# Performance work log

Measured on AMD Instinct MI355X. Metric: run time of the kernel, lower is better.

The kernel has to match this reference:

```python
import jax, jax.numpy as jnp
import numpy as np

B, U, L, H = 2048, 512, 32, 64  # batch, num_units, latent_dim, hidden


def setup_inputs() -> dict:
    key = jax.random.key(0)
    ks = jax.random.split(key, 17)
    s = 0.05  # weight scale
    inp = {
        "x": jax.random.normal(ks[0], (B, U), dtype=jnp.float32),
        # encoder: U -> 64 -> 64 -> 64 -> L
        "We1": jax.random.normal(ks[1], (U, H), jnp.float32) * s,
        "be1": jnp.zeros((H,), jnp.float32),
        "We2": jax.random.normal(ks[2], (H, H), jnp.float32) * s,
        "be2": jnp.zeros((H,), jnp.float32),
        "We3": jax.random.normal(ks[3], (H, H), jnp.float32) * s,
        "be3": jnp.zeros((H,), jnp.float32),
        "We4": jax.random.normal(ks[4], (H, L), jnp.float32) * s,
        "be4": jnp.zeros((L,), jnp.float32),
        # U disjoint decoders, weights stacked along unit axis: L -> 64 -> 64 -> 64 -> 1
        "Wd1": jax.random.normal(ks[5], (U, L, H), jnp.float32) * s,
        "bd1": jnp.zeros((U, H), jnp.float32),
        "Wd2": jax.random.normal(ks[6], (U, H, H), jnp.float32) * s,
        "bd2": jnp.zeros((U, H), jnp.float32),
        "Wd3": jax.random.normal(ks[7], (U, H, H), jnp.float32) * s,
        "bd3": jnp.zeros((U, H), jnp.float32),
        "Wd4": jax.random.normal(ks[8], (U, H), jnp.float32) * s,  # last layer out_dim=1, squeezed
        "bd4": jnp.zeros((U,), jnp.float32),
    }
    return inp


def reference(x, We1, be1, We2, be2, We3, be3, We4, be4,
              Wd1, bd1, Wd2, bd2, Wd3, bd3, Wd4, bd4):
    # shared encoder MLP: [B, U] -> [B, L]
    z = jax.nn.relu(x @ We1 + be1)
    z = jax.nn.relu(z @ We2 + be2)
    z = jax.nn.relu(z @ We3 + be3)
    z = z @ We4 + be4  # [B, L]
    # all U decoders batched as grouped GEMMs: [B, L] -> [B, U]
    h = jax.nn.relu(jnp.einsum('bl,ulh->buh', z, Wd1) + bd1)   # [B, U, H]
    h = jax.nn.relu(jnp.einsum('buh,uhk->buk', h, Wd2) + bd2)  # [B, U, H]
    h = jax.nn.relu(jnp.einsum('buh,uhk->buk', h, Wd3) + bd3)  # [B, U, H]
    out = jnp.einsum('buh,uh->bu', h, Wd4) + bd4               # [B, U]
    return out
```

## Files before the change

kernel.cpp:

```cpp
#include <hip/hip_runtime.h>
#include <hip/hip_bf16.h>
#include <hip/hip_fp16.h>
#include <stdint.h>

#define NB 2048
#define NU 512
#define NL 32
#define NH 64

typedef float    f4    __attribute__((ext_vector_type(4)));
typedef uint32_t u32x4 __attribute__((ext_vector_type(4)));
typedef _Float16 h8    __attribute__((ext_vector_type(8)));
typedef _Float16 h2    __attribute__((ext_vector_type(2)));

__device__ __forceinline__ f4 mfma16h(u32x4 a, u32x4 b, f4 c) {
    return __builtin_amdgcn_mfma_f32_16x16x32_f16(
        __builtin_bit_cast(h8, a), __builtin_bit_cast(h8, b), c, 0, 0, 0);
}

__device__ __forceinline__ uint32_t pk2h(float a, float b) {
    uint32_t la = (uint32_t)__half_as_ushort(__float2half_rn(a));
    uint32_t hb = (uint32_t)__half_as_ushort(__float2half_rn(b));
    return la | (hb << 16);
}

__device__ __forceinline__ uint32_t pk_rtz(float e, float o) {
    return __builtin_bit_cast(uint32_t, __builtin_amdgcn_cvt_pkrtz(e, o));
}

__device__ __forceinline__ uint32_t pk_relu(float e, float o) {
    uint32_t r = pk_rtz(e, o);
    asm("v_pk_max_f16 %0, %1, 0" : "=v"(r) : "v"(r));
    return r;
}

__device__ __forceinline__ float dot2(uint32_t a, uint32_t b, float c) {
    return __builtin_amdgcn_fdot2(__builtin_bit_cast(h2, a),
                                  __builtin_bit_cast(h2, b), c, false);
}

__global__ __launch_bounds__(512)
void enc_kernel(const float* __restrict__ x,
                const float* __restrict__ We1, const float* __restrict__ be1,
                const float* __restrict__ We2, const float* __restrict__ be2,
                const float* __restrict__ We3, const float* __restrict__ be3,
                const float* __restrict__ We4, const float* __restrict__ be4,
                uint32_t* __restrict__ zpk)
{
    const int RE = 8;
    __shared__ float xs[RE][512];
    __shared__ float ws[128 * 64];
    __shared__ float h[RE][NH];
    __shared__ float h2s[RE][NH];

    const int t  = threadIdx.x;
    const int r0 = blockIdx.x * RE;

    {
        const f4* xv  = (const f4*)(x + (size_t)r0 * 512);
        f4*       xsv = (f4*)&xs[0][0];
        for (int i = t; i < RE * 512 / 4; i += 512) xsv[i] = xv[i];
    }

    const int j = t & 63;
    const int w = t >> 6;

    float acc0 = be1[j];
    for (int kc = 0; kc < 512; kc += 128) {
        __syncthreads();
        const f4* wv  = (const f4*)(We1 + (size_t)kc * 64);
        f4*       wsv = (f4*)ws;
        for (int i = t; i < 128 * 64 / 4; i += 512) wsv[i] = wv[i];
        __syncthreads();
        #pragma unroll 8
        for (int k = 0; k < 128; ++k)
            acc0 = fmaf(xs[w][kc + k], ws[k * 64 + j], acc0);
    }
    acc0 = fmaxf(acc0, 0.f);
    __syncthreads();
    h[w][j] = acc0;
    __syncthreads();

    acc0 = be2[j];
    #pragma unroll
    for (int k = 0; k < 64; ++k)
        acc0 = fmaf(h[w][k], We2[k * 64 + j], acc0);
    acc0 = fmaxf(acc0, 0.f);
    h2s[w][j] = acc0;
    __syncthreads();

    acc0 = be3[j];
    #pragma unroll
    for (int k = 0; k < 64; ++k)
        acc0 = fmaf(h2s[w][k], We3[k * 64 + j], acc0);
    acc0 = fmaxf(acc0, 0.f);
    h[w][j] = acc0;
    __syncthreads();

    if (t < 256) {
        const int j4  = t & 31;
        const int row = t >> 5;
        float acc = be4[j4];
        #pragma unroll
        for (int k = 0; k < 64; ++k)
            acc = fmaf(h[row][k], We4[k * 32 + j4], acc);
        float nb = __shfl_xor(acc, 1);
        if ((j4 & 1) == 0)
            zpk[(size_t)(r0 + row) * 16 + (j4 >> 1)] = pk2h(acc, nb);
    }
}

template <int K2>
__device__ __forceinline__ void stageW(const float* __restrict__ g,
                                       uint32_t (*dst)[68], int t)
{
    for (int g4 = t; g4 < K2 * 16; g4 += 256) {
        const int k2 = g4 >> 4, c4 = (g4 & 15) << 2;
        f4 a = *(const f4*)(g + (size_t)(2 * k2) * NH + c4);
        f4 b = *(const f4*)(g + (size_t)(2 * k2 + 1) * NH + c4);
        u32x4 p;
        p[0] = pk2h(a[0], b[0]);
        p[1] = pk2h(a[1], b[1]);
        p[2] = pk2h(a[2], b[2]);
        p[3] = pk2h(a[3], b[3]);
        *(u32x4*)&dst[k2][c4] = p;
    }
}

__global__ __launch_bounds__(256)
void dec_kernel(const uint32_t* __restrict__ zpk,
                const float* __restrict__ Wd1, const float* __restrict__ bd1,
                const float* __restrict__ Wd2, const float* __restrict__ bd2,
                const float* __restrict__ Wd3, const float* __restrict__ bd3,
                const float* __restrict__ Wd4, const float* __restrict__ bd4,
                float* __restrict__ out)
{
    __shared__ uint32_t wpk1[16][68];
    __shared__ uint32_t wpk2[32][68];
    __shared__ uint32_t wpk3[72][68];
    __shared__ float bsh[3][NH];
    __shared__ float w4s[NH];

    const int bid  = blockIdx.x;
    const int half = bid >> 9;
    const int ub   = bid & 511;
    const int u = ((ub & 7) << 4) | (((ub >> 3) & 3) << 7) | (ub >> 5);
    const int t = threadIdx.x;

    stageW<16>(Wd1 + (size_t)u * NL * NH, wpk1, t);
    stageW<32>(Wd2 + (size_t)u * NH * NH, wpk2, t);
    stageW<32>(Wd3 + (size_t)u * NH * NH, wpk3, t);
    if (t < NH) {
        bsh[0][t] = bd1[(size_t)u * NH + t];
        bsh[1][t] = bd2[(size_t)u * NH + t];
        bsh[2][t] = bd3[(size_t)u * NH + t];
        w4s[t]    = Wd4[(size_t)u * NH + t];
    }
    __syncthreads();

    const int w  = t >> 6;
    const int lr = t & 15;
    const int lg = (t & 63) >> 4;
    const float b4 = bd4[u];

    int cperm[4];
    #pragma unroll
    for (int mt = 0; mt < 4; ++mt)
        cperm[mt] = ((mt >> 1) << 5) + ((lr >> 2) << 3) + ((mt & 1) << 2) + (lr & 3);

    u32x4 a1[4], a2[4][2], a3[4][2];
    #pragma unroll
    for (int mt = 0; mt < 4; ++mt) {
        const int c = cperm[mt];
        #pragma unroll
        for (int i = 0; i < 4; ++i)
            a1[mt][i] = wpk1[lg * 4 + i][c];
        #pragma unroll
        for (int ks = 0; ks < 2; ++ks) {
            #pragma unroll
            for (int i = 0; i < 4; ++i) {
                a2[mt][ks][i] = wpk2[ks * 16 + lg * 4 + i][c];
                a3[mt][ks][i] = wpk3[ks * 16 + lg * 4 + i][c];
            }
        }
    }

    int bq[4];
    #pragma unroll
    for (int mt = 0; mt < 4; ++mt)
        bq[mt] = ((mt >> 1) << 5) + (lg << 3) + ((mt & 1) << 2);

    f4 bc1[4], bc2[4], bc3[4];
    #pragma unroll
    for (int mt = 0; mt < 4; ++mt) {
        bc1[mt] = *(const f4*)&bsh[0][bq[mt]];
        bc2[mt] = *(const f4*)&bsh[1][bq[mt]];
        bc3[mt] = *(const f4*)&bsh[2][bq[mt]];
    }

    uint32_t wd4pk[4][2];
    #pragma unroll
    for (int mt = 0; mt < 4; ++mt) {
        wd4pk[mt][0] = pk2h(w4s[bq[mt]],     w4s[bq[mt] + 1]);
        wd4pk[mt][1] = pk2h(w4s[bq[mt] + 2], w4s[bq[mt] + 3]);
    }

    const int rl  = w * 16 + lr;
    const int it0 = half * 8;

    u32x4 zc[2];
    zc[0] = *(const u32x4*)(zpk + (size_t)(it0 * 128 + rl) * 16 + lg * 4);
    zc[1] = *(const u32x4*)(zpk + (size_t)(it0 * 128 + 64 + rl) * 16 + lg * 4);

    for (int it = it0; it < it0 + 8; ++it) {
        const int rb  = it * 128 + rl;
        const int rbn = (it0 + ((it - it0 + 1) & 7)) * 128 + rl;
        u32x4 zn[2];
        zn[0] = *(const u32x4*)(zpk + (size_t)rbn * 16 + lg * 4);
        zn[1] = *(const u32x4*)(zpk + (size_t)(rbn + 64) * 16 + lg * 4);

        f4 acc[2][4];

        #pragma unroll
        for (int s = 0; s < 2; ++s)
            #pragma unroll
            for (int mt = 0; mt < 4; ++mt)
                acc[s][mt] = mfma16h(a1[mt], zc[s], bc1[mt]);

        u32x4 bf0[2], bf1[2];
        #pragma unroll
        for (int s = 0; s < 2; ++s) {
            bf0[s][0] = pk_relu(acc[s][0][0], acc[s][0][1]);
            bf0[s][1] = pk_relu(acc[s][0][2], acc[s][0][3]);
            bf0[s][2] = pk_relu(acc[s][1][0], acc[s][1][1]);
            bf0[s][3] = pk_relu(acc[s][1][2], acc[s][1][3]);
            bf1[s][0] = pk_relu(acc[s][2][0], acc[s][2][1]);
            bf1[s][1] = pk_relu(acc[s][2][2], acc[s][2][3]);
            bf1[s][2] = pk_relu(acc[s][3][0], acc[s][3][1]);
            bf1[s][3] = pk_relu(acc[s][3][2], acc[s][3][3]);
        }

        #pragma unroll
        for (int s = 0; s < 2; ++s)
            #pragma unroll
            for (int mt = 0; mt < 4; ++mt)
                acc[s][mt] = mfma16h(a2[mt][0], bf0[s], bc2[mt]);
        #pragma unroll
        for (int s = 0; s < 2; ++s)
            #pragma unroll
            for (int mt = 0; mt < 4; ++mt)
                acc[s][mt] = mfma16h(a2[mt][1], bf1[s], acc[s][mt]);

        #pragma unroll
        for (int s = 0; s < 2; ++s) {
            bf0[s][0] = pk_relu(acc[s][0][0], acc[s][0][1]);
            bf0[s][1] = pk_relu(acc[s][0][2], acc[s][0][3]);
            bf0[s][2] = pk_relu(acc[s][1][0], acc[s][1][1]);
            bf0[s][3] = pk_relu(acc[s][1][2], acc[s][1][3]);
            bf1[s][0] = pk_relu(acc[s][2][0], acc[s][2][1]);
            bf1[s][1] = pk_relu(acc[s][2][2], acc[s][2][3]);
            bf1[s][2] = pk_relu(acc[s][3][0], acc[s][3][1]);
            bf1[s][3] = pk_relu(acc[s][3][2], acc[s][3][3]);
        }

        #pragma unroll
        for (int s = 0; s < 2; ++s)
            #pragma unroll
            for (int mt = 0; mt < 4; ++mt)
                acc[s][mt] = mfma16h(a3[mt][0], bf0[s], bc3[mt]);
        #pragma unroll
        for (int s = 0; s < 2; ++s)
            #pragma unroll
            for (int mt = 0; mt < 4; ++mt)
                acc[s][mt] = mfma16h(a3[mt][1], bf1[s], acc[s][mt]);

        #pragma unroll
        for (int s = 0; s < 2; ++s) {
            float pa = 0.f, pb = 0.f;
            #pragma unroll
            for (int mt = 0; mt < 4; ++mt) {
                uint32_t p0 = pk_relu(acc[s][mt][0], acc[s][mt][1]);
                uint32_t p1 = pk_relu(acc[s][mt][2], acc[s][mt][3]);
                pa = dot2(p0, wd4pk[mt][0], pa);
                pb = dot2(p1, wd4pk[mt][1], pb);
            }
            float part = pa + pb;
            part += __shfl_xor(part, 16);
            part += __shfl_xor(part, 32);
            if ((t & 48) == 0)
                out[(size_t)(rb + s * 64) * NU + u] = part + b4;
        }

        zc[0] = zn[0]; zc[1] = zn[1];
    }
}

extern "C" void kernel_launch(void* const* d_in, const int* in_sizes, int n_in,
                              void* d_out, int out_size, void* d_ws, size_t ws_size,
                              hipStream_t stream)
{
    const float* x   = (const float*)d_in[0];
    const float* We1 = (const float*)d_in[1];
    const float* be1 = (const float*)d_in[2];
    const float* We2 = (const float*)d_in[3];
    const float* be2 = (const float*)d_in[4];
    const float* We3 = (const float*)d_in[5];
    const float* be3 = (const float*)d_in[6];
    const float* We4 = (const float*)d_in[7];
    const float* be4 = (const float*)d_in[8];
    const float* Wd1 = (const float*)d_in[9];
    const float* bd1 = (const float*)d_in[10];
    const float* Wd2 = (const float*)d_in[11];
    const float* bd2 = (const float*)d_in[12];
    const float* Wd3 = (const float*)d_in[13];
    const float* bd3 = (const float*)d_in[14];
    const float* Wd4 = (const float*)d_in[15];
    const float* bd4 = (const float*)d_in[16];
    float* out = (float*)d_out;

    uint32_t* zpk = (uint32_t*)d_ws;

    enc_kernel<<<NB / 8, 512, 0, stream>>>(x, We1, be1, We2, be2, We3, be3,
                                           We4, be4, zpk);
    dec_kernel<<<NU * 2, 256, 0, stream>>>(zpk, Wd1, bd1, Wd2, bd2,
                                           Wd3, bd3, Wd4, bd4, out);
}
```

Before: 47.65 us.

## Process full batch per unit block with four row slabs and permlane reductions

The decoder grid drops from two blocks per unit to one block per unit, and each iteration processes four 64-row slabs instead of two, so each unit's weights are staged once. Bias registers are now reloaded from LDS inside the loop rather than kept live. The cross-lane reduction uses permlane16/32 swap instructions instead of shuffles. The wpk3 shared array is enlarged, which raises LDS per block and lowers occupancy. Halving the grid reduces parallelism across CUs on a 512-block launch.

```diff
diff --git a/kernel.cpp b/kernel.cpp
--- a/kernel.cpp
+++ b/kernel.cpp
@@ -37,6 +37,15 @@
 __device__ __forceinline__ float dot2(uint32_t a, uint32_t b, float c) {
     return __builtin_amdgcn_fdot2(__builtin_bit_cast(h2, a),
                                   __builtin_bit_cast(h2, b), c, false);
+}
+
+__device__ __forceinline__ float red_lg(float x) {
+    float a = x, b = x;
+    asm("v_permlane16_swap_b32 %0, %1" : "+v"(a), "+v"(b));
+    x = a + b;
+    a = x; b = x;
+    asm("v_permlane32_swap_b32 %0, %1" : "+v"(a), "+v"(b));
+    return a + b;
 }
 
 __global__ __launch_bounds__(512)
@@ -137,14 +146,12 @@
 {
     __shared__ uint32_t wpk1[16][68];
     __shared__ uint32_t wpk2[32][68];
-    __shared__ uint32_t wpk3[72][68];
+    __shared__ uint32_t wpk3[150][68];
     __shared__ float bsh[3][NH];
     __shared__ float w4s[NH];
 
-    const int bid  = blockIdx.x;
-    const int half = bid >> 9;
-    const int ub   = bid & 511;
-    const int u = ((ub & 7) << 4) | (((ub >> 3) & 3) << 7) | (ub >> 5);
+    const int bid = blockIdx.x;
+    const int u = ((bid & 7) << 4) | (((bid >> 3) & 3) << 7) | (bid >> 5);
     const int t = threadIdx.x;
 
     stageW<16>(Wd1 + (size_t)u * NL * NH, wpk1, t);
@@ -190,14 +197,6 @@
     for (int mt = 0; mt < 4; ++mt)
         bq[mt] = ((mt >> 1) << 5) + (lg << 3) + ((mt & 1) << 2);
 
-    f4 bc1[4], bc2[4], bc3[4];
-    #pragma unroll
-    for (int mt = 0; mt < 4; ++mt) {
-        bc1[mt] = *(const f4*)&bsh[0][bq[mt]];
-        bc2[mt] = *(const f4*)&bsh[1][bq[mt]];
-        bc3[mt] = *(const f4*)&bsh[2][bq[mt]];
-    }
-
     uint32_t wd4pk[4][2];
     #pragma unroll
     for (int mt = 0; mt < 4; ++mt) {
@@ -205,77 +204,82 @@
         wd4pk[mt][1] = pk2h(w4s[bq[mt] + 2], w4s[bq[mt] + 3]);
     }
 
-    const int rl  = w * 16 + lr;
-    const int it0 = half * 8;
-
-    u32x4 zc[2];
-    zc[0] = *(const u32x4*)(zpk + (size_t)(it0 * 128 + rl) * 16 + lg * 4);
-    zc[1] = *(const u32x4*)(zpk + (size_t)(it0 * 128 + 64 + rl) * 16 + lg * 4);
-
-    for (int it = it0; it < it0 + 8; ++it) {
-        const int rb  = it * 128 + rl;
-        const int rbn = (it0 + ((it - it0 + 1) & 7)) * 128 + rl;
-        u32x4 zn[2];
-        zn[0] = *(const u32x4*)(zpk + (size_t)rbn * 16 + lg * 4);
-        zn[1] = *(const u32x4*)(zpk + (size_t)(rbn + 64) * 16 + lg * 4);
-
-        f4 acc[2][4];
-
-        #pragma unroll
-        for (int s = 0; s < 2; ++s)
+    const int rl = w * 16 + lr;
+
+    u32x4 zc[4];
+    #pragma unroll
+    for (int s = 0; s < 4; ++s)
+        zc[s] = *(const u32x4*)(zpk + (size_t)(rl + s * 64) * 16 + lg * 4);
+
+    for (int it = 0; it < 8; ++it) {
+        const int rb  = it * 256 + rl;
+        const int rbn = ((it + 1) & 7) * 256 + rl;
+
+        f4 acc[4][4];
+
+        {
+            f4 c0 = *(const f4*)&bsh[0][bq[0]];
+            f4 c1 = *(const f4*)&bsh[0][bq[1]];
+            f4 c2 = *(const f4*)&bsh[0][bq[2]];
+            f4 c3 = *(const f4*)&bsh[0][bq[3]];
+            #pragma unroll
+            for (int s = 0; s < 4; ++s) {
+                acc[s][0] = mfma16h(a1[0], zc[s], c0);
+                acc[s][1] = mfma16h(a1[1], zc[s], c1);
+                acc[s][2] = mfma16h(a1[2], zc[s], c2);
+                acc[s][3] = mfma16h(a1[3], zc[s], c3);
+            }
+        }
+
+        u32x4 zn[4];
+        #pragma unroll
+        for (int s = 0; s < 4; ++s)
+            zn[s] = *(const u32x4*)(zpk + (size_t)(rbn + s * 64) * 16 + lg * 4);
+
+        f4 bc2[4], bc3[4];
+        #pragma unroll
+        for (int mt = 0; mt < 4; ++mt) {
+            bc2[mt] = *(const f4*)&bsh[1][bq[mt]];
+            bc3[mt] = *(const f4*)&bsh[2][bq[mt]];
+        }
+        #pragma unroll
+        for (int s = 0; s < 4; ++s) {
+            u32x4 bf0, bf1;
+            bf0[0] = pk_relu(acc[s][0][0], acc[s][0][1]);
+            bf0[1] = pk_relu(acc[s][0][2], acc[s][0][3]);
+            bf0[2] = pk_relu(acc[s][1][0], acc[s][1][1]);
+            bf0[3] = pk_relu(acc[s][1][2], acc[s][1][3]);
+            bf1[0] = pk_relu(acc[s][2][0], acc[s][2][1]);
+            bf1[1] = pk_relu(acc[s][2][2], acc[s][2][3]);
+            bf1[2] = pk_relu(acc[s][3][0], acc[s][3][1]);
+            bf1[3] = pk_relu(acc[s][3][2], acc[s][3][3]);
+
             #pragma unroll
             for (int mt = 0; mt < 4; ++mt)
-                acc[s][mt] = mfma16h(a1[mt], zc[s], bc1[mt]);
-
-        u32x4 bf0[2], bf1[2];
-        #pragma unroll
-        for (int s = 0; s < 2; ++s) {
-            bf0[s][0] = pk_relu(acc[s][0][0], acc[s][0][1]);
-            bf0[s][1] = pk_relu(acc[s][0][2], acc[s][0][3]);
-            bf0[s][2] = pk_relu(acc[s][1][0], acc[s][1][1]);
-            bf0[s][3] = pk_relu(acc[s][1][2], acc[s][1][3]);
-            bf1[s][0] = pk_relu(acc[s][2][0], acc[s][2][1]);
-            bf1[s][1] = pk_relu(acc[s][2][2], acc[s][2][3]);
-            bf1[s][2] = pk_relu(acc[s][3][0], acc[s][3][1]);
-            bf1[s][3] = pk_relu(acc[s][3][2], acc[s][3][3]);
-        }
-
-        #pragma unroll
-        for (int s = 0; s < 2; ++s)
+                acc[s][mt] = mfma16h(a2[mt][0], bf0, bc2[mt]);
             #pragma unroll
             for (int mt = 0; mt < 4; ++mt)
-                acc[s][mt] = mfma16h(a2[mt][0], bf0[s], bc2[mt]);
-        #pragma unroll
-        for (int s = 0; s < 2; ++s)
+                acc[s][mt] = mfma16h(a2[mt][1], bf1, acc[s][mt]);
+
+            bf0[0] = pk_relu(acc[s][0][0], acc[s][0][1]);
+            bf0[1] = pk_relu(acc[s][0][2], acc[s][0][3]);
+            bf0[2] = pk_relu(acc[s][1][0], acc[s][1][1]);
+            bf0[3] = pk_relu(acc[s][1][2], acc[s][1][3]);
+            bf1[0] = pk_relu(acc[s][2][0], acc[s][2][1]);
+            bf1[1] = pk_relu(acc[s][2][2], acc[s][2][3]);
+            bf1[2] = pk_relu(acc[s][3][0], acc[s][3][1]);
+            bf1[3] = pk_relu(acc[s][3][2], acc[s][3][3]);
+
             #pragma unroll
             for (int mt = 0; mt < 4; ++mt)
-                acc[s][mt] = mfma16h(a2[mt][1], bf1[s], acc[s][mt]);
-
-        #pragma unroll
-        for (int s = 0; s < 2; ++s) {
-            bf0[s][0] = pk_relu(acc[s][0][0], acc[s][0][1]);
-            bf0[s][1] = pk_relu(acc[s][0][2], acc[s][0][3]);
-            bf0[s][2] = pk_relu(acc[s][1][0], acc[s][1][1]);
-            bf0[s][3] = pk_relu(acc[s][1][2], acc[s][1][3]);
-            bf1[s][0] = pk_relu(acc[s][2][0], acc[s][2][1]);
-            bf1[s][1] = pk_relu(acc[s][2][2], acc[s][2][3]);
-            bf1[s][2] = pk_relu(acc[s][3][0], acc[s][3][1]);
-            bf1[s][3] = pk_relu(acc[s][3][2], acc[s][3][3]);
-        }
-
-        #pragma unroll
-        for (int s = 0; s < 2; ++s)
+                acc[s][mt] = mfma16h(a3[mt][0], bf0, bc3[mt]);
             #pragma unroll
             for (int mt = 0; mt < 4; ++mt)
-                acc[s][mt] = mfma16h(a3[mt][0], bf0[s], bc3[mt]);
-        #pragma unroll
-        for (int s = 0; s < 2; ++s)
-            #pragma unroll
-            for (int mt = 0; mt < 4; ++mt)
-                acc[s][mt] = mfma16h(a3[mt][1], bf1[s], acc[s][mt]);
-
-        #pragma unroll
-        for (int s = 0; s < 2; ++s) {
+                acc[s][mt] = mfma16h(a3[mt][1], bf1, acc[s][mt]);
+        }
+
+        #pragma unroll
+        for (int s = 0; s < 4; ++s) {
             float pa = 0.f, pb = 0.f;
             #pragma unroll
             for (int mt = 0; mt < 4; ++mt) {
@@ -284,14 +288,13 @@
                 pa = dot2(p0, wd4pk[mt][0], pa);
                 pb = dot2(p1, wd4pk[mt][1], pb);
             }
-            float part = pa + pb;
-            part += __shfl_xor(part, 16);
-            part += __shfl_xor(part, 32);
+            float part = red_lg(pa + pb);
             if ((t & 48) == 0)
                 out[(size_t)(rb + s * 64) * NU + u] = part + b4;
         }
 
-        zc[0] = zn[0]; zc[1] = zn[1];
+        #pragma unroll
+        for (int s = 0; s < 4; ++s) zc[s] = zn[s];
     }
 }
 
@@ -322,6 +325,6 @@
 
     enc_kernel<<<NB / 8, 512, 0, stream>>>(x, We1, be1, We2, be2, We3, be3,
                                            We4, be4, zpk);
-    dec_kernel<<<NU * 2, 256, 0, stream>>>(zpk, Wd1, bd1, Wd2, bd2,
-                                           Wd3, bd3, Wd4, bd4, out);
-}
+    dec_kernel<<<NU, 256, 0, stream>>>(zpk, Wd1, bd1, Wd2, bd2,
+                                       Wd3, bd3, Wd4, bd4, out);
+}
```

New measurement: 44.59 us, median of 2. 6.4% less time.
